# Kernel optimization log

Hardware: AMD Instinct MI355X
Metric: run time of the kernel (lower is better)

The kernel has to match this reference:

```python
import jax, jax.numpy as jnp
import numpy as np

D_MODEL = 2048
N_HEADS = 16
N_KV = 4
D_HEAD = D_MODEL // N_HEADS  # 128
KERNEL = 4
TOTAL_QKV = (N_HEADS + 2 * N_KV) * D_HEAD  # 3072
BATCH, SEQ = 2, 2048


def setup_inputs() -> dict:
    key = jax.random.key(0)
    ks = jax.random.split(key, 6)
    s = 1.0 / np.sqrt(D_MODEL)
    return {
        "hidden_states": jax.random.normal(ks[0], (BATCH, SEQ, D_MODEL), jnp.float32),
        "w_q": jax.random.normal(ks[1], (D_MODEL, N_HEADS * D_HEAD), jnp.float32) * s,
        "w_k": jax.random.normal(ks[2], (D_MODEL, N_KV * D_HEAD), jnp.float32) * s,
        "w_v": jax.random.normal(ks[3], (D_MODEL, N_KV * D_HEAD), jnp.float32) * s,
        "w_o": jax.random.normal(ks[4], (N_HEADS * D_HEAD, D_MODEL), jnp.float32) * s,
        "conv_w": jax.random.normal(ks[5], (TOTAL_QKV, KERNEL), jnp.float32) * 0.1,
    }


def _canon_b(x, conv_w):
    """Depthwise causal conv1d with residual. x: [B,S,C], conv_w: [C,K]."""
    K = conv_w.shape[1]
    xp = jnp.pad(x, ((0, 0), (K - 1, 0), (0, 0)))  # left pad for causality
    S = x.shape[1]
    out = sum(xp[:, k:k + S, :] * conv_w[:, k] for k in range(K))
    return x + out


def reference(hidden_states, w_q, w_k, w_v, w_o, conv_w):
    B, S, _ = hidden_states.shape
    q = hidden_states @ w_q   # [B,S,Hq*Dh]
    k = hidden_states @ w_k   # [B,S,Hkv*Dh]
    v = hidden_states @ w_v
    qkv = jnp.concatenate([q, k, v], axis=-1)
    qkv = _canon_b(qkv, conv_w)
    q_dim = N_HEADS * D_HEAD
    kv_dim = N_KV * D_HEAD
    q, k, v = jnp.split(qkv, [q_dim, q_dim + kv_dim], axis=-1)
    q = q.reshape(B, S, N_HEADS, D_HEAD)
    k = k.reshape(B, S, N_KV, D_HEAD)
    v = v.reshape(B, S, N_KV, D_HEAD)
    # GQA: repeat kv heads to match query heads
    groups = N_HEADS // N_KV
    k = jnp.repeat(k, groups, axis=2)
    v = jnp.repeat(v, groups, axis=2)
    scale = 1.0 / np.sqrt(D_HEAD)
    scores = jnp.einsum("bqhd,bkhd->bhqk", q, k) * scale  # [B,H,S,S]
    causal = jnp.tril(jnp.ones((S, S), dtype=bool))
    scores = jnp.where(causal, scores, jnp.finfo(scores.dtype).min)
    probs = jax.nn.softmax(scores, axis=-1)
    attended = jnp.einsum("bhqk,bkhd->bqhd", probs, v)  # [B,S,H,Dh]
    attended = attended.reshape(B, S, N_HEADS * D_HEAD)
    return attended @ w_o
```

## Files before the change

### kernel.cpp

```cpp
#include <hip/hip_runtime.h>
#include <stdint.h>

typedef unsigned short u16;
typedef short short8 __attribute__((ext_vector_type(8)));
typedef float f32x4 __attribute__((ext_vector_type(4)));
typedef float f32x16 __attribute__((ext_vector_type(16)));

#define DM    2048
#define NH    16
#define NKV   4
#define DH    128
#define TQKV  3072
#define NB    2
#define SEQL  2048
#define MROWS (NB * SEQL)
#define QDIM  (NH * DH)
#define KVDIM (NKV * DH)
#define QSCALE_L2E 0.1275174336f

#define MFMA16(a, b, c) __builtin_amdgcn_mfma_f32_16x16x32_bf16((a), (b), (c), 0, 0, 0)
#define MFMA32(a, b, c) __builtin_amdgcn_mfma_f32_32x32x16_bf16((a), (b), (c), 0, 0, 0)

__device__ __forceinline__ u16 f2bf(float f) {
  uint32_t u = __float_as_uint(f);
  u += 0x7fffu + ((u >> 16) & 1u);
  return (u16)(u >> 16);
}
__device__ __forceinline__ float bf2f(u16 h) {
  return __uint_as_float(((uint32_t)h) << 16);
}
__device__ __forceinline__ void gload16(const u16* g, u16* l) {
  __builtin_amdgcn_global_load_lds((__attribute__((address_space(1))) void*)(u16*)g,
                                   (__attribute__((address_space(3))) void*)l, 16, 0, 0);
}
__device__ __forceinline__ uint32_t cvtpk(float lo, float hi) {
  uint32_t r;
  asm("v_cvt_pk_bf16_f32 %0, %1, %2" : "=v"(r) : "v"(lo), "v"(hi));
  return r;
}
__device__ __forceinline__ void swapln(uint32_t& a, uint32_t& b) {
  asm volatile("v_permlane32_swap_b32 %0, %1" : "+v"(a), "+v"(b));
}

__global__ void k_f32_to_bf16(const float* __restrict__ src, u16* __restrict__ dst, int n) {
  int i = (blockIdx.x * blockDim.x + threadIdx.x) * 4;
  if (i >= n) return;
  float4 v = *reinterpret_cast<const float4*>(src + i);
  u16 o0 = f2bf(v.x), o1 = f2bf(v.y), o2 = f2bf(v.z), o3 = f2bf(v.w);
  u16* d = dst + i;
  d[0] = o0; d[1] = o1; d[2] = o2; d[3] = o3;
}

__global__ void k_transpose_f32_bf16(const float* __restrict__ src, u16* __restrict__ dst,
                                     int K, int N, int rowOff, int dstLd) {
  __shared__ float t[32][33];
  const int n0 = blockIdx.x * 32, k0 = blockIdx.y * 32;
  const int tx = threadIdx.x, ty = threadIdx.y;
#pragma unroll
  for (int i = ty; i < 32; i += 8)
    t[i][tx] = src[(size_t)(k0 + i) * N + (n0 + tx)];
  __syncthreads();
#pragma unroll
  for (int i = ty; i < 32; i += 8)
    dst[(size_t)(rowOff + n0 + i) * dstLd + (k0 + tx)] = f2bf(t[tx][i]);
}

__global__ void k_transpose_bf16(const u16* __restrict__ src, u16* __restrict__ dst, int R, int C) {
  __shared__ u16 t[32][33];
  const size_t zoff = (size_t)blockIdx.z * R * C;
  const int c0 = blockIdx.x * 32, r0 = blockIdx.y * 32;
  const int tx = threadIdx.x, ty = threadIdx.y;
#pragma unroll
  for (int i = ty; i < 32; i += 8)
    t[i][tx] = src[zoff + (size_t)(r0 + i) * C + (c0 + tx)];
  __syncthreads();
#pragma unroll
  for (int i = ty; i < 32; i += 8)
    dst[zoff + (size_t)(c0 + i) * R + (r0 + tx)] = t[tx][i];
}

template <int OUTBF>
__global__ __launch_bounds__(256) void k_gemm_bt(const u16* __restrict__ A, const u16* __restrict__ Bt,
                                                 float* __restrict__ Cf, u16* __restrict__ Cb,
                                                 int M, int N, int K) {
  __shared__ u16 As[2][128 * 32];
  __shared__ u16 Bs[2][128 * 32];
  const int tid = threadIdx.x;
  const int m0 = blockIdx.x * 128;
  const int n0 = blockIdx.y * 128;
  const int r  = tid >> 2;
  const int c8 = (tid & 3) << 3;
  const u16* Ag0 = A  + (size_t)(m0 + r) * K + c8;
  const u16* Ag1 = A  + (size_t)(m0 + 64 + r) * K + c8;
  const u16* Bg0 = Bt + (size_t)(n0 + r) * K + c8;
  const u16* Bg1 = Bt + (size_t)(n0 + 64 + r) * K + c8;

  auto stage = [&](int buf, int kt) {
    const int kg = kt * 32;
    gload16(Ag0 + kg, &As[buf][tid * 8]);
    gload16(Ag1 + kg, &As[buf][2048 + tid * 8]);
    gload16(Bg0 + kg, &Bs[buf][tid * 8]);
    gload16(Bg1 + kg, &Bs[buf][2048 + tid * 8]);
  };

  f32x4 acc[4][4];
#pragma unroll
  for (int i = 0; i < 4; ++i)
#pragma unroll
    for (int j = 0; j < 4; ++j) acc[i][j] = (f32x4){0.f, 0.f, 0.f, 0.f};

  const int wv = tid >> 6, ln = tid & 63;
  const int wr = (wv >> 1) * 64, wc = (wv & 1) * 64;
  const int lr = ln & 15, lko = (ln >> 4) * 8;

  stage(0, 0);
  __syncthreads();

  const int nk = K >> 5;
  for (int kt = 0; kt < nk; ++kt) {
    const int cur = kt & 1;
    if (kt + 1 < nk) stage(cur ^ 1, kt + 1);
    short8 af[4], bf[4];
#pragma unroll
    for (int i = 0; i < 4; ++i)
      af[i] = *reinterpret_cast<const short8*>(&As[cur][(wr + i * 16 + lr) * 32 + lko]);
#pragma unroll
    for (int i = 0; i < 4; ++i)
      bf[i] = *reinterpret_cast<const short8*>(&Bs[cur][(wc + i * 16 + lr) * 32 + lko]);
#pragma unroll
    for (int i = 0; i < 4; ++i)
#pragma unroll
      for (int j = 0; j < 4; ++j)
        acc[i][j] = MFMA16(af[i], bf[j], acc[i][j]);
    __syncthreads();
  }

  const int rg = (ln >> 4) * 4;
#pragma unroll
  for (int i = 0; i < 4; ++i) {
#pragma unroll
    for (int j = 0; j < 4; ++j) {
      const int row = m0 + wr + i * 16 + rg;
      const int col = n0 + wc + j * 16 + lr;
#pragma unroll
      for (int q = 0; q < 4; ++q) {
        float v = acc[i][j][q];
        if (OUTBF) Cb[(size_t)(row + q) * N + col] = f2bf(v);
        else       Cf[(size_t)(row + q) * N + col] = v;
      }
    }
  }
}

__global__ void k_conv_route(const u16* __restrict__ qkv, const float* __restrict__ cw,
                             u16* __restrict__ Qh, u16* __restrict__ Kh, u16* __restrict__ Vsd) {
  const int row = blockIdx.x;
  const int b = row >> 11, s = row & 2047;
  const int c = threadIdx.x * 8;
  float x[4][8];
#pragma unroll
  for (int k = 0; k < 4; ++k) {
    const int sr = s + k - 3;
    if (sr < 0) {
#pragma unroll
      for (int j = 0; j < 8; ++j) x[k][j] = 0.f;
    } else {
      short8 v = *reinterpret_cast<const short8*>(&qkv[(size_t)(b * SEQL + sr) * TQKV + c]);
#pragma unroll
      for (int j = 0; j < 8; ++j) x[k][j] = bf2f((u16)v[j]);
    }
  }
  float o[8];
#pragma unroll
  for (int j = 0; j < 8; ++j) {
    float4 w4 = *reinterpret_cast<const float4*>(&cw[(c + j) * 4]);
    o[j] = x[3][j] + x[0][j] * w4.x + x[1][j] * w4.y + x[2][j] * w4.z + x[3][j] * w4.w;
  }
  short8 ov;
  if (c < QDIM) {
#pragma unroll
    for (int j = 0; j < 8; ++j) ov[j] = (short)f2bf(o[j] * QSCALE_L2E);
    const int h = c >> 7, d = c & 127;
    *reinterpret_cast<short8*>(&Qh[((size_t)(b * NH + h) * SEQL + s) * DH + d]) = ov;
  } else if (c < QDIM + KVDIM) {
#pragma unroll
    for (int j = 0; j < 8; ++j) ov[j] = (short)f2bf(o[j]);
    const int cc = c - QDIM;
    const int h = cc >> 7, d = cc & 127;
    *reinterpret_cast<short8*>(&Kh[((size_t)(b * NKV + h) * SEQL + s) * DH + d]) = ov;
  } else {
#pragma unroll
    for (int j = 0; j < 8; ++j) ov[j] = (short)f2bf(o[j]);
    const int cc = c - QDIM - KVDIM;
    const int h = cc >> 7, d = cc & 127;
    *reinterpret_cast<short8*>(&Vsd[((size_t)(b * NKV + h) * SEQL + s) * DH + d]) = ov;
  }
}

__global__ __launch_bounds__(512) void k_attn(const u16* __restrict__ Qh, const u16* __restrict__ Kh,
                                              const u16* __restrict__ Vt, u16* __restrict__ att,
                                              u16* __restrict__ pO, float* __restrict__ pm,
                                              float* __restrict__ pl) {
  static const int qb_tab[12] = {7,7,3,6,6,5,5,2,4,4,1,0};
  static const int t0_tab[12] = {0,16,0,0,14,0,12,0,0,10,0,0};
  static const int t1_tab[12] = {16,32,16,14,28,12,24,12,10,20,8,4};
  static const int sp_tab[12] = {1,1,0,1,1,1,1,0,1,1,0,0};
  static const int ch_tab[12] = {0,1,0,0,1,0,1,0,0,1,0,0};

  const int ii = blockIdx.x >> 5;
  const int bh = blockIdx.x & 31;
  const int qb = qb_tab[ii];
  const int tA = t0_tab[ii], tB = t1_tab[ii];
  const int split = sp_tab[ii], chk = ch_tab[ii];
  const int s = bh & 7, tt = bh >> 3;
  const int b = s >> 2, kvh = s & 3;
  const int h = kvh * 4 + tt;
  const int bhl = b * NH + h;

  __shared__ u16 Ks[2][64 * 128];
  __shared__ u16 Vs[2][128 * 64];
  const int tid = threadIdx.x, wv = tid >> 6, ln = tid & 63;
  const int lq = ln & 31, hi = ln >> 5;
  const int hi16 = hi * 16;
  const int q0w = qb * 256 + wv * 32;
  const int qg = q0w + lq;
  const int swr = (lq & 7) << 4;

  const u16* qrow = Qh + ((size_t)(b * NH + h) * SEQL + qg) * DH;
  short8 qf[8];
#pragma unroll
  for (int dblk = 0; dblk < 8; ++dblk)
    qf[dblk] = *reinterpret_cast<const short8*>(qrow + dblk * 16 + hi * 8);

  const u16* kg = Kh + (size_t)(b * NKV + kvh) * SEQL * DH;
  const u16* vg = Vt + (size_t)(b * NKV + kvh) * DH * SEQL;

  const int ck0 = tid, ck1 = tid + 512;
  const int krow0 = ck0 >> 4, kcb0 = (ck0 & 15) << 4;
  const int krow1 = ck1 >> 4, kcb1 = (ck1 & 15) << 4;
  const int koff0 = krow0 * DH + ((kcb0 ^ ((krow0 & 7) << 4)) >> 1);
  const int koff1 = krow1 * DH + ((kcb1 ^ ((krow1 & 7) << 4)) >> 1);
  const int vd0 = ck0 >> 3, vcb0 = (ck0 & 7) << 4;
  const int vd1 = ck1 >> 3, vcb1 = (ck1 & 7) << 4;
  const int voff0 = vd0 * SEQL + ((vcb0 ^ ((vd0 & 7) << 4)) >> 1);
  const int voff1 = vd1 * SEQL + ((vcb1 ^ ((vd1 & 7) << 4)) >> 1);

  auto stage = [&](int buf, int kvs) {
    gload16(kg + (size_t)kvs * DH + koff0, &Ks[buf][ck0 * 8]);
    gload16(kg + (size_t)kvs * DH + koff1, &Ks[buf][ck1 * 8]);
    gload16(vg + (size_t)kvs + voff0, &Vs[buf][ck0 * 8]);
    gload16(vg + (size_t)kvs + voff1, &Vs[buf][ck1 * 8]);
  };

  f32x16 oacc[4];
#pragma unroll
  for (int nb = 0; nb < 4; ++nb)
#pragma unroll
    for (int rq = 0; rq < 16; ++rq) oacc[nb][rq] = 0.f;
  float mrow = -1e30f, lrow = 0.f;

  stage(0, tA * 64);
  __syncthreads();

  for (int t = tA; t < tB; ++t) {
    const int cur = (t - tA) & 1;
    const int kvs = t * 64;
    if (t + 1 < tB) stage(cur ^ 1, kvs + 64);
    if (kvs <= q0w + 31) {
      const u16* ks = Ks[cur];
      const u16* vs = Vs[cur];
      f32x16 st[2];
#pragma unroll
      for (int kvb = 0; kvb < 2; ++kvb)
#pragma unroll
        for (int rq = 0; rq < 16; ++rq) st[kvb][rq] = 0.f;

      __builtin_amdgcn_s_setprio(1);
#pragma unroll
      for (int kvb = 0; kvb < 2; ++kvb) {
        const u16* krow = ks + (kvb * 32 + lq) * 128;
#pragma unroll
        for (int dblk = 0; dblk < 8; ++dblk) {
          short8 kf = *reinterpret_cast<const short8*>(krow + (((dblk * 32 + hi16) ^ swr) >> 1));
          st[kvb] = MFMA32(kf, qf[dblk], st[kvb]);
        }
      }
      __builtin_amdgcn_s_setprio(0);

      if (kvs + 63 > q0w) {
#pragma unroll
        for (int kvb = 0; kvb < 2; ++kvb)
#pragma unroll
          for (int rq = 0; rq < 16; ++rq) {
            const int kvg = kvs + kvb * 32 + (rq & 3) + 8 * (rq >> 2) + 4 * hi;
            if (kvg > qg) st[kvb][rq] = -1e30f;
          }
      }

      float a0 = st[0][0], a1 = st[0][1], a2 = st[0][2], a3 = st[0][3];
#pragma unroll
      for (int kvb = 0; kvb < 2; ++kvb)
#pragma unroll
        for (int rq = (kvb ? 0 : 4); rq < 16; rq += 4) {
          a0 = fmaxf(a0, st[kvb][rq]);
          a1 = fmaxf(a1, st[kvb][rq + 1]);
          a2 = fmaxf(a2, st[kvb][rq + 2]);
          a3 = fmaxf(a3, st[kvb][rq + 3]);
        }
      float tm = fmaxf(fmaxf(a0, a1), fmaxf(a2, a3));
      tm = fmaxf(tm, __shfl_xor(tm, 32));
      if (__any(tm > mrow + 11.0f)) {
        const float nm = fmaxf(mrow, tm);
        const float scl = exp2f(mrow - nm);
        mrow = nm;
        lrow *= scl;
#pragma unroll
        for (int nb = 0; nb < 4; ++nb)
#pragma unroll
          for (int rq = 0; rq < 16; ++rq) oacc[nb][rq] *= scl;
      }
      float s0 = 0.f, s1 = 0.f, s2 = 0.f, s3 = 0.f;
#pragma unroll
      for (int kvb = 0; kvb < 2; ++kvb)
#pragma unroll
        for (int rq = 0; rq < 16; rq += 4) {
          float p0 = exp2f(st[kvb][rq] - mrow);
          float p1 = exp2f(st[kvb][rq + 1] - mrow);
          float p2 = exp2f(st[kvb][rq + 2] - mrow);
          float p3 = exp2f(st[kvb][rq + 3] - mrow);
          st[kvb][rq] = p0; st[kvb][rq + 1] = p1; st[kvb][rq + 2] = p2; st[kvb][rq + 3] = p3;
          s0 += p0; s1 += p1; s2 += p2; s3 += p3;
        }
      float ps = (s0 + s1) + (s2 + s3);
      ps += __shfl_xor(ps, 32);
      lrow += ps;

      uint32_t w[4][4];
#pragma unroll
      for (int kvb = 0; kvb < 2; ++kvb) {
        uint32_t x0 = cvtpk(st[kvb][0], st[kvb][1]);
        uint32_t y0 = cvtpk(st[kvb][4], st[kvb][5]);
        swapln(x0, y0);
        uint32_t x1 = cvtpk(st[kvb][2], st[kvb][3]);
        uint32_t y1 = cvtpk(st[kvb][6], st[kvb][7]);
        swapln(x1, y1);
        w[kvb * 2][0] = x0; w[kvb * 2][1] = x1; w[kvb * 2][2] = y0; w[kvb * 2][3] = y1;
        uint32_t x2 = cvtpk(st[kvb][8], st[kvb][9]);
        uint32_t y2 = cvtpk(st[kvb][12], st[kvb][13]);
        swapln(x2, y2);
        uint32_t x3 = cvtpk(st[kvb][10], st[kvb][11]);
        uint32_t y3 = cvtpk(st[kvb][14], st[kvb][15]);
        swapln(x3, y3);
        w[kvb * 2 + 1][0] = x2; w[kvb * 2 + 1][1] = x3; w[kvb * 2 + 1][2] = y2; w[kvb * 2 + 1][3] = y3;
      }
      short8 pa[4];
#pragma unroll
      for (int kc = 0; kc < 4; ++kc) {
        union { uint32_t uw[4]; short8 s; } pu;
#pragma unroll
        for (int j = 0; j < 4; ++j) pu.uw[j] = w[kc][j];
        pa[kc] = pu.s;
      }

      __builtin_amdgcn_s_setprio(1);
#pragma unroll
      for (int nb = 0; nb < 4; ++nb) {
        const u16* vrow = vs + (nb * 32 + lq) * 64;
#pragma unroll
        for (int kc = 0; kc < 4; ++kc) {
          short8 vf = *reinterpret_cast<const short8*>(vrow + (((kc * 32 + hi16) ^ swr) >> 1));
          oacc[nb] = MFMA32(vf, pa[kc], oacc[nb]);
        }
      }
      __builtin_amdgcn_s_setprio(0);
    }
    __syncthreads();
  }

  if (!split) {
    const float inv = 1.0f / lrow;
    u16* orow = att + ((size_t)(b * SEQL + qg)) * QDIM + h * DH;
#pragma unroll
    for (int nb = 0; nb < 4; ++nb)
#pragma unroll
      for (int rg = 0; rg < 4; ++rg) {
        const int rq = rg * 4;
        uint2 vout;
        vout.x = cvtpk(oacc[nb][rq] * inv, oacc[nb][rq + 1] * inv);
        vout.y = cvtpk(oacc[nb][rq + 2] * inv, oacc[nb][rq + 3] * inv);
        *reinterpret_cast<uint2*>(orow + nb * 32 + 8 * rg + 4 * hi) = vout;
      }
  } else {
    const int rowp = ((bhl * 4 + (qb - 4)) << 8) + wv * 32 + lq;
    u16* prow = pO + (size_t)chk * 32768 * 128 + (size_t)rowp * 128;
#pragma unroll
    for (int nb = 0; nb < 4; ++nb)
#pragma unroll
      for (int rg = 0; rg < 4; ++rg) {
        const int rq = rg * 4;
        uint2 vout;
        vout.x = cvtpk(oacc[nb][rq], oacc[nb][rq + 1]);
        vout.y = cvtpk(oacc[nb][rq + 2], oacc[nb][rq + 3]);
        *reinterpret_cast<uint2*>(prow + nb * 32 + 8 * rg + 4 * hi) = vout;
      }
    if (!hi) {
      pm[chk * 32768 + rowp] = mrow;
      pl[chk * 32768 + rowp] = lrow;
    }
  }
}

__global__ void k_combine(const u16* __restrict__ pO, const float* __restrict__ pm,
                          const float* __restrict__ pl, u16* __restrict__ att) {
  const int e = blockIdx.x * 256 + threadIdx.x;
  const int rowp = e >> 4;
  const int d8 = (e & 15) * 8;
  const float m0 = pm[rowp], m1 = pm[32768 + rowp];
  const float l0 = pl[rowp], l1 = pl[32768 + rowp];
  const float mm = fmaxf(m0, m1);
  const float a0 = exp2f(m0 - mm), a1 = exp2f(m1 - mm);
  const float inv = 1.0f / (l0 * a0 + l1 * a1);
  const float w0 = a0 * inv, w1 = a1 * inv;
  short8 o0 = *reinterpret_cast<const short8*>(pO + (size_t)rowp * 128 + d8);
  short8 o1 = *reinterpret_cast<const short8*>(pO + (size_t)32768 * 128 + (size_t)rowp * 128 + d8);
  const int bh = rowp >> 10, qb = 4 + ((rowp >> 8) & 3), r = rowp & 255;
  const int b = bh >> 4, h = bh & 15;
  u16* orow = att + ((size_t)(b * SEQL + qb * 256 + r)) * QDIM + h * DH + d8;
  uint2 vout;
  float r0 = bf2f((u16)o0[0]) * w0 + bf2f((u16)o1[0]) * w1;
  float r1 = bf2f((u16)o0[1]) * w0 + bf2f((u16)o1[1]) * w1;
  float r2 = bf2f((u16)o0[2]) * w0 + bf2f((u16)o1[2]) * w1;
  float r3 = bf2f((u16)o0[3]) * w0 + bf2f((u16)o1[3]) * w1;
  float r4 = bf2f((u16)o0[4]) * w0 + bf2f((u16)o1[4]) * w1;
  float r5 = bf2f((u16)o0[5]) * w0 + bf2f((u16)o1[5]) * w1;
  float r6 = bf2f((u16)o0[6]) * w0 + bf2f((u16)o1[6]) * w1;
  float r7 = bf2f((u16)o0[7]) * w0 + bf2f((u16)o1[7]) * w1;
  vout.x = ((uint32_t)f2bf(r1) << 16) | f2bf(r0);
  vout.y = ((uint32_t)f2bf(r3) << 16) | f2bf(r2);
  uint2 vout2;
  vout2.x = ((uint32_t)f2bf(r5) << 16) | f2bf(r4);
  vout2.y = ((uint32_t)f2bf(r7) << 16) | f2bf(r6);
  *reinterpret_cast<uint2*>(orow) = vout;
  *reinterpret_cast<uint2*>(orow + 4) = vout2;
}

extern "C" void kernel_launch(void* const* d_in, const int* in_sizes, int n_in,
                              void* d_out, int out_size, void* d_ws, size_t ws_size,
                              hipStream_t stream) {
  const float* hin = (const float*)d_in[0];
  const float* wq  = (const float*)d_in[1];
  const float* wk  = (const float*)d_in[2];
  const float* wvv = (const float*)d_in[3];
  const float* wo  = (const float*)d_in[4];
  const float* cw  = (const float*)d_in[5];
  float* out = (float*)d_out;
  char* ws = (char*)d_ws;

  u16* h_bf = (u16*)(ws + 0);
  u16* Wt   = (u16*)(ws + 16777216);
  u16* Wot  = (u16*)(ws + 29360128);
  u16* Qh   = (u16*)(ws + 37748736);
  u16* Kh   = (u16*)(ws + 54525952);
  u16* Vsd  = (u16*)(ws + 58720256);
  u16* Vt   = (u16*)(ws + 62914560);
  u16* att  = (u16*)(ws + 67108864);
  u16* qkv  = (u16*)d_out;
  u16*   pO = (u16*)d_out;
  float* pm = (float*)((char*)d_out + 16777216);
  float* pl = (float*)((char*)d_out + 16777216 + 262144);

  dim3 tb(32, 8);
  k_f32_to_bf16<<<8192, 256, 0, stream>>>(hin, h_bf, MROWS * DM);
  k_transpose_f32_bf16<<<dim3(64, 64), tb, 0, stream>>>(wq, Wt, 2048, 2048, 0, 2048);
  k_transpose_f32_bf16<<<dim3(16, 64), tb, 0, stream>>>(wk, Wt, 2048, 512, 2048, 2048);
  k_transpose_f32_bf16<<<dim3(16, 64), tb, 0, stream>>>(wvv, Wt, 2048, 512, 2560, 2048);
  k_transpose_f32_bf16<<<dim3(64, 64), tb, 0, stream>>>(wo, Wot, 2048, 2048, 0, 2048);
  k_gemm_bt<1><<<dim3(32, 24), 256, 0, stream>>>(h_bf, Wt, nullptr, qkv, MROWS, TQKV, DM);
  k_conv_route<<<MROWS, 384, 0, stream>>>(qkv, cw, Qh, Kh, Vsd);
  k_transpose_bf16<<<dim3(4, 64, NB * NKV), tb, 0, stream>>>(Vsd, Vt, SEQL, DH);
  k_attn<<<dim3(384), 512, 0, stream>>>(Qh, Kh, Vt, att, pO, pm, pl);
  k_combine<<<dim3(2048), 256, 0, stream>>>(pO, pm, pl, att);
  k_gemm_bt<0><<<dim3(32, 16), 256, 0, stream>>>(att, Wot, out, nullptr, MROWS, DM, DM);
}
```

Before: 245.1 us.

## Replace GEMM with 256x256-tile, 8-wave kernel using swizzled LDS and staged prefetch

Both projection GEMMs now use a new kernel with 256x256 output tiles, 512 threads, a BK of 64, and an XOR-swizzled LDS layout. Global-to-LDS loads for the next k-tile are split into quarters and interleaved between four MFMA phases, with explicit vmcnt waits, raw barriers and setprio. The aim is more data reuse per LDS byte, fewer bank conflicts and better overlap of loads with compute. The cost is far fewer blocks: 192 for the QKV GEMM and 128 for the output GEMM, which may underfill the 256 CUs.

```diff
diff --git a/kernel.cpp b/kernel.cpp
--- a/kernel.cpp
+++ b/kernel.cpp
@@ -41,6 +41,10 @@
 __device__ __forceinline__ void swapln(uint32_t& a, uint32_t& b) {
   asm volatile("v_permlane32_swap_b32 %0, %1" : "+v"(a), "+v"(b));
 }
+__device__ __forceinline__ void barrier_raw() {
+  __builtin_amdgcn_s_barrier();
+  asm volatile("" ::: "memory");
+}
 
 __global__ void k_f32_to_bf16(const float* __restrict__ src, u16* __restrict__ dst, int n) {
   int i = (blockIdx.x * blockDim.x + threadIdx.x) * 4;
@@ -80,76 +84,157 @@
 }
 
 template <int OUTBF>
-__global__ __launch_bounds__(256) void k_gemm_bt(const u16* __restrict__ A, const u16* __restrict__ Bt,
+__global__ __launch_bounds__(512) void k_gemm256(const u16* __restrict__ A, const u16* __restrict__ Bt,
                                                  float* __restrict__ Cf, u16* __restrict__ Cb,
                                                  int M, int N, int K) {
-  __shared__ u16 As[2][128 * 32];
-  __shared__ u16 Bs[2][128 * 32];
+  __shared__ u16 lds[65536];
   const int tid = threadIdx.x;
-  const int m0 = blockIdx.x * 128;
-  const int n0 = blockIdx.y * 128;
-  const int r  = tid >> 2;
-  const int c8 = (tid & 3) << 3;
-  const u16* Ag0 = A  + (size_t)(m0 + r) * K + c8;
-  const u16* Ag1 = A  + (size_t)(m0 + 64 + r) * K + c8;
-  const u16* Bg0 = Bt + (size_t)(n0 + r) * K + c8;
-  const u16* Bg1 = Bt + (size_t)(n0 + 64 + r) * K + c8;
-
-  auto stage = [&](int buf, int kt) {
-    const int kg = kt * 32;
-    gload16(Ag0 + kg, &As[buf][tid * 8]);
-    gload16(Ag1 + kg, &As[buf][2048 + tid * 8]);
-    gload16(Bg0 + kg, &Bs[buf][tid * 8]);
-    gload16(Bg1 + kg, &Bs[buf][2048 + tid * 8]);
+  const int m0 = blockIdx.x * 256, n0 = blockIdx.y * 256;
+  const int wv = tid >> 6, ln = tid & 63;
+  const int wm = wv >> 2, wn = wv & 3;
+  const int lr = ln & 15, lg4 = ln >> 4;
+  const int rdo = lr * 32 + ((lg4 * 8) ^ (((lr >> 3) & 1) << 4));
+
+  int rS[2], cS[2], ck8[2];
+#pragma unroll
+  for (int j = 0; j < 2; ++j) {
+    const int ck = tid + j * 512;
+    const int rr = (ck >> 2) & 15;
+    const int cc = ((ck & 3) * 8) ^ (((rr >> 3) & 1) << 4);
+    const int s = ck >> 6;
+    rS[j] = (s >> 1) * 16 + rr;
+    cS[j] = (s & 1) * 32 + cc;
+    ck8[j] = ck * 8;
+  }
+
+  auto stA = [&](int buf, int h, int kt) {
+#pragma unroll
+    for (int j = 0; j < 2; ++j)
+      gload16(A + (size_t)(m0 + h * 128 + rS[j]) * K + kt * 64 + cS[j],
+              &lds[buf * 32768 + h * 8192 + ck8[j]]);
   };
-
-  f32x4 acc[4][4];
-#pragma unroll
-  for (int i = 0; i < 4; ++i)
-#pragma unroll
-    for (int j = 0; j < 4; ++j) acc[i][j] = (f32x4){0.f, 0.f, 0.f, 0.f};
-
-  const int wv = tid >> 6, ln = tid & 63;
-  const int wr = (wv >> 1) * 64, wc = (wv & 1) * 64;
-  const int lr = ln & 15, lko = (ln >> 4) * 8;
-
-  stage(0, 0);
-  __syncthreads();
-
-  const int nk = K >> 5;
-  for (int kt = 0; kt < nk; ++kt) {
-    const int cur = kt & 1;
-    if (kt + 1 < nk) stage(cur ^ 1, kt + 1);
-    short8 af[4], bf[4];
+  auto stB = [&](int buf, int h, int kt) {
+#pragma unroll
+    for (int j = 0; j < 2; ++j)
+      gload16(Bt + (size_t)(n0 + h * 128 + rS[j]) * K + kt * 64 + cS[j],
+              &lds[buf * 32768 + 16384 + h * 8192 + ck8[j]]);
+  };
+
+  f32x4 acc[2][2][4][2];
+#pragma unroll
+  for (int qm = 0; qm < 2; ++qm)
+#pragma unroll
+    for (int qn = 0; qn < 2; ++qn)
+#pragma unroll
+      for (int i = 0; i < 4; ++i)
+#pragma unroll
+        for (int j = 0; j < 2; ++j) acc[qm][qn][i][j] = (f32x4){0.f, 0.f, 0.f, 0.f};
+
+  const int nk = K >> 6;
+  stA(0, 0, 0); stB(0, 0, 0); stA(0, 1, 0); stB(0, 1, 0);
+  if (nk > 1) stA(1, 0, 1);
+
+  for (int t = 0; t < nk; ++t) {
+    const int buf = t & 1, nb = buf ^ 1;
+    const u16* Ab = &lds[buf * 32768 + wm * 8192];
+    const u16* Bb = &lds[buf * 32768 + 16384 + (wn >> 1) * 8192];
+    short8 af[4][2], bf[2][2], bf2[2][2];
+
+    if (t + 1 < nk) {
+      stB(nb, 0, t + 1);
+      asm volatile("s_waitcnt vmcnt(4)" ::: "memory");
+    } else {
+      asm volatile("s_waitcnt vmcnt(0)" ::: "memory");
+    }
+    barrier_raw();
 #pragma unroll
     for (int i = 0; i < 4; ++i)
-      af[i] = *reinterpret_cast<const short8*>(&As[cur][(wr + i * 16 + lr) * 32 + lko]);
+#pragma unroll
+      for (int kk = 0; kk < 2; ++kk)
+        af[i][kk] = *reinterpret_cast<const short8*>(&Ab[(i * 2 + kk) * 512 + rdo]);
+#pragma unroll
+    for (int j = 0; j < 2; ++j)
+#pragma unroll
+      for (int kk = 0; kk < 2; ++kk)
+        bf[j][kk] = *reinterpret_cast<const short8*>(&Bb[(((wn & 1) * 4 + j) * 2 + kk) * 512 + rdo]);
+    __builtin_amdgcn_s_setprio(1);
 #pragma unroll
     for (int i = 0; i < 4; ++i)
-      bf[i] = *reinterpret_cast<const short8*>(&Bs[cur][(wc + i * 16 + lr) * 32 + lko]);
+#pragma unroll
+      for (int j = 0; j < 2; ++j)
+#pragma unroll
+        for (int kk = 0; kk < 2; ++kk)
+          acc[0][0][i][j] = MFMA16(af[i][kk], bf[j][kk], acc[0][0][i][j]);
+    __builtin_amdgcn_s_setprio(0);
+    barrier_raw();
+
+#pragma unroll
+    for (int j = 0; j < 2; ++j)
+#pragma unroll
+      for (int kk = 0; kk < 2; ++kk)
+        bf2[j][kk] = *reinterpret_cast<const short8*>(&Bb[(((wn & 1) * 4 + 2 + j) * 2 + kk) * 512 + rdo]);
+    if (t + 1 < nk) stA(nb, 1, t + 1);
+    barrier_raw();
+    __builtin_amdgcn_s_setprio(1);
 #pragma unroll
     for (int i = 0; i < 4; ++i)
 #pragma unroll
-      for (int j = 0; j < 4; ++j)
-        acc[i][j] = MFMA16(af[i], bf[j], acc[i][j]);
-    __syncthreads();
-  }
-
-  const int rg = (ln >> 4) * 4;
-#pragma unroll
-  for (int i = 0; i < 4; ++i) {
-#pragma unroll
-    for (int j = 0; j < 4; ++j) {
-      const int row = m0 + wr + i * 16 + rg;
-      const int col = n0 + wc + j * 16 + lr;
-#pragma unroll
-      for (int q = 0; q < 4; ++q) {
-        float v = acc[i][j][q];
-        if (OUTBF) Cb[(size_t)(row + q) * N + col] = f2bf(v);
-        else       Cf[(size_t)(row + q) * N + col] = v;
-      }
-    }
-  }
+      for (int j = 0; j < 2; ++j)
+#pragma unroll
+        for (int kk = 0; kk < 2; ++kk)
+          acc[0][1][i][j] = MFMA16(af[i][kk], bf2[j][kk], acc[0][1][i][j]);
+    __builtin_amdgcn_s_setprio(0);
+    barrier_raw();
+
+#pragma unroll
+    for (int i = 0; i < 4; ++i)
+#pragma unroll
+      for (int kk = 0; kk < 2; ++kk)
+        af[i][kk] = *reinterpret_cast<const short8*>(&Ab[((4 + i) * 2 + kk) * 512 + rdo]);
+    if (t + 1 < nk) stB(nb, 1, t + 1);
+    barrier_raw();
+    __builtin_amdgcn_s_setprio(1);
+#pragma unroll
+    for (int i = 0; i < 4; ++i)
+#pragma unroll
+      for (int j = 0; j < 2; ++j)
+#pragma unroll
+        for (int kk = 0; kk < 2; ++kk)
+          acc[1][0][i][j] = MFMA16(af[i][kk], bf[j][kk], acc[1][0][i][j]);
+    __builtin_amdgcn_s_setprio(0);
+    barrier_raw();
+
+    if (t + 2 < nk) stA(buf, 0, t + 2);
+    barrier_raw();
+    __builtin_amdgcn_s_setprio(1);
+#pragma unroll
+    for (int i = 0; i < 4; ++i)
+#pragma unroll
+      for (int j = 0; j < 2; ++j)
+#pragma unroll
+        for (int kk = 0; kk < 2; ++kk)
+          acc[1][1][i][j] = MFMA16(af[i][kk], bf2[j][kk], acc[1][1][i][j]);
+    __builtin_amdgcn_s_setprio(0);
+    barrier_raw();
+  }
+
+#pragma unroll
+  for (int qm = 0; qm < 2; ++qm)
+#pragma unroll
+    for (int qn = 0; qn < 2; ++qn)
+#pragma unroll
+      for (int i = 0; i < 4; ++i)
+#pragma unroll
+        for (int j = 0; j < 2; ++j) {
+          const int row = m0 + wm * 128 + qm * 64 + i * 16 + lg4 * 4;
+          const int col = n0 + wn * 64 + qn * 32 + j * 16 + lr;
+#pragma unroll
+          for (int q = 0; q < 4; ++q) {
+            float v = acc[qm][qn][i][j][q];
+            if (OUTBF) Cb[(size_t)(row + q) * N + col] = f2bf(v);
+            else       Cf[(size_t)(row + q) * N + col] = v;
+          }
+        }
 }
 
 __global__ void k_conv_route(const u16* __restrict__ qkv, const float* __restrict__ cw,
@@ -475,10 +560,10 @@
   k_transpose_f32_bf16<<<dim3(16, 64), tb, 0, stream>>>(wk, Wt, 2048, 512, 2048, 2048);
   k_transpose_f32_bf16<<<dim3(16, 64), tb, 0, stream>>>(wvv, Wt, 2048, 512, 2560, 2048);
   k_transpose_f32_bf16<<<dim3(64, 64), tb, 0, stream>>>(wo, Wot, 2048, 2048, 0, 2048);
-  k_gemm_bt<1><<<dim3(32, 24), 256, 0, stream>>>(h_bf, Wt, nullptr, qkv, MROWS, TQKV, DM);
+  k_gemm256<1><<<dim3(16, 12), 512, 0, stream>>>(h_bf, Wt, nullptr, qkv, MROWS, TQKV, DM);
   k_conv_route<<<MROWS, 384, 0, stream>>>(qkv, cw, Qh, Kh, Vsd);
   k_transpose_bf16<<<dim3(4, 64, NB * NKV), tb, 0, stream>>>(Vsd, Vt, SEQL, DH);
   k_attn<<<dim3(384), 512, 0, stream>>>(Qh, Kh, Vt, att, pO, pm, pl);
   k_combine<<<dim3(2048), 256, 0, stream>>>(pO, pm, pl, att);
-  k_gemm_bt<0><<<dim3(32, 16), 256, 0, stream>>>(att, Wot, out, nullptr, MROWS, DM, DM);
-}
+  k_gemm256<0><<<dim3(16, 8), 512, 0, stream>>>(att, Wot, out, nullptr, MROWS, DM, DM);
+}
```

After: 258.4 us. 1.05x slower.
